# Kernel tuning notes

Measured on AMD Instinct MI355X. Metric: run time of the kernel, lower is better.

Reference implementation:

```python
import jax, jax.numpy as jnp
import numpy as np

B, N, FIN = 64, 128, 768
NFEAT, NHID, NHEADS, NCLASS = 1024, 512, 8, 512
ALPHA = 0.2
NEG_E = -9e15
NEG_S = -9e10


def setup_inputs():
    rng = np.random.RandomState(0)
    x = rng.randn(B, N, FIN).astype(np.float32)
    offset_mapping = np.zeros((B, N, 2), dtype=np.int32)
    attention_mask = np.zeros((B, N), dtype=np.float32)
    tag = np.zeros((B, N), dtype=np.float32)
    for b in range(B):
        pos, k, groups = 1, 0, 0
        n_words = int(rng.randint(30, 60))
        for _ in range(n_words):
            wl = int(rng.randint(1, 4))
            if k + wl > 120:
                break
            for _t in range(wl):
                offset_mapping[b, k] = (pos, pos + 2)  # contiguous inside word
                pos += 2
                k += 1
            pos += 1  # 1-char gap => word boundary: end == next_start - 1
            groups += 1
        groups -= 1  # last word is never closed (matches torch loop semantics)
        attention_mask[b, :groups] = 1.0
        tag[b, :groups] = (rng.rand(groups) > 0.1).astype(np.float32)
        tag[b, 0] = 1.0
    adj = (rng.rand(B, N, N) < 0.3).astype(np.float32)
    adj = np.clip(adj + np.eye(N, dtype=np.float32)[None], 0.0, 1.0)
    s = 0.02
    p = {
        'Wg_w': s * rng.randn(FIN, NFEAT), 'Wg_b': np.zeros(NFEAT),
        'hW_w': s * rng.randn(NHEADS, NFEAT, NHID), 'hW_b': np.zeros((NHEADS, NHID)),
        'ha_w': s * rng.randn(NHEADS, 2 * NHID), 'ha_b': np.zeros(NHEADS),
        'oW_w': s * rng.randn(NHID * NHEADS, NCLASS), 'oW_b': np.zeros(NCLASS),
        'oa_w': s * rng.randn(2 * NCLASS), 'oa_b': np.zeros(()),
        'fin_w': s * rng.randn(NCLASS, 1), 'fin_b': np.zeros(1),
    }
    inp = {
        'x': jnp.asarray(x), 'tag': jnp.asarray(tag),
        'offset_mapping': jnp.asarray(offset_mapping),
        'attention_mask': jnp.asarray(attention_mask), 'adj': jnp.asarray(adj),
    }
    for kk, vv in p.items():
        inp[kk] = jnp.asarray(np.asarray(vv, dtype=np.float32))
    return inp


def _group_pool(x, offs):
    # Vectorized form of the offset-grouped mean pooling loop.
    zero = (offs[:, :, 0] == 0) & (offs[:, :, 1] == 0)  # padding rows
    fz = jnp.argmax(zero, axis=1)                       # first padding row (break)
    pos = jnp.arange(N)
    valid = pos[None, :] < fz[:, None]
    nxt_start = jnp.concatenate([offs[:, 1:, 0], jnp.zeros((offs.shape[0], 1), offs.dtype)], axis=1)
    boundary = valid & (offs[:, :, 1] == nxt_start - 1)
    bi = boundary.astype(jnp.int32)
    cs = jnp.cumsum(bi, axis=1)
    seg = cs - bi                 # exclusive cumsum: group id per token
    G = cs[:, -1]                 # number of closed groups per row

    def per(xb, segb, bb):
        sums = jax.ops.segment_sum(xb, segb, num_segments=N + 1)[:N]
        cnts = jax.ops.segment_sum(jnp.ones((N,), xb.dtype), segb, num_segments=N + 1)[:N]
        ends = jax.ops.segment_sum((jnp.arange(N) + 1) * bb, segb, num_segments=N + 1)[:N]
        return sums, cnts, ends

    sums, cnts, ends = jax.vmap(per)(x, seg, bi)
    g = jnp.arange(N)[None, :]
    gv = g < G[:, None]
    x_off = jnp.where(gv[..., None], sums / jnp.maximum(cnts, 1.0)[..., None], 0.0)
    starts = jnp.concatenate([jnp.zeros((offs.shape[0], 1), jnp.int32), ends[:, :-1]], axis=1)
    starts = jnp.where(gv, starts, 0)
    ends = jnp.where(gv, ends, 0)
    return x_off, jnp.stack([starts, ends], axis=-1)  # [B,N,F_in], [B,N,2]


def _expand_row(fix):
    # Flatten [start,end) ranges in order until the first [0,0] row; rest = arange.
    zr = (fix[:, 0] == 0) & (fix[:, 1] == 0)
    fz = jnp.argmax(zr)
    valid = jnp.arange(N) < fz
    lens = jnp.where(valid, fix[:, 1] - fix[:, 0], 0)
    csum = jnp.cumsum(lens)
    excl = csum - lens
    total = csum[-1]
    l = jnp.arange(N)
    k = jnp.clip(jnp.searchsorted(csum, l, side='right'), 0, N - 1)
    val = fix[k, 0] + (l - excl[k])
    return jnp.where(l < total, val, l)


def _scores(x_off, tag, attention_mask, adj, Wg_w, Wg_b, hW_w, hW_b, ha_w, ha_b, oW_w, oW_b, oa_w, oa_b, fin_w, fin_b):
    xw = x_off @ Wg_w + Wg_b                                    # [B,N,NFEAT]
    h = jnp.einsum('bnf,hfo->bhno', xw, hW_w) + hW_b[None, :, None, :]
    # e_ij = leakyrelu(a1.h_i + a2.h_j + b): decomposition of a([h_i||h_j])
    e = jax.nn.leaky_relu(
        jnp.einsum('bhno,ho->bhn', h, ha_w[:, :NHID])[:, :, :, None]
        + jnp.einsum('bhno,ho->bhn', h, ha_w[:, NHID:])[:, :, None, :]
        + ha_b[None, :, None, None], ALPHA)
    att = jax.nn.softmax(jnp.where(adj[:, None, :, :] > 0, e, NEG_E), axis=-1)
    x1 = jax.nn.elu(jnp.einsum('bhij,bhjo->bhio', att, h))
    x1 = x1.transpose(0, 2, 1, 3).reshape(x1.shape[0], N, NHEADS * NHID)
    h2 = x1 @ oW_w + oW_b
    e2 = jax.nn.leaky_relu((h2 @ oa_w[:NCLASS])[:, :, None]
                           + (h2 @ oa_w[NCLASS:])[:, None, :] + oa_b, ALPHA)
    att2 = jax.nn.softmax(jnp.where(adj > 0, e2, NEG_E), axis=-1)
    x2 = jax.nn.elu(jnp.einsum('bij,bjo->bio', att2, h2))
    logits = (x2 @ fin_w + fin_b)[..., 0]                        # [B,N]
    m = jnp.where(tag > 0, attention_mask, 0.0)
    sc = jax.nn.softmax(jnp.where(m > 0, logits * m, NEG_S), axis=1)
    summary = m.sum(axis=1)
    ii = (jnp.arange(N, 0, -1).astype(jnp.float32)[None, :] / summary[:, None]) * m
    ii = jax.nn.softmax(jnp.where(m > 0, ii, NEG_S), axis=1)
    return sc + ii


def reference(x, tag, offset_mapping, attention_mask, adj, Wg_w, Wg_b, hW_w, hW_b, ha_w, ha_b, oW_w, oW_b, oa_w, oa_b, fin_w, fin_b):
    x_off, index_group = _group_pool(x, offset_mapping)
    sc = _scores(x_off, tag, attention_mask, adj, Wg_w, Wg_b, hW_w, hW_b, ha_w, ha_b, oW_w, oW_b, oa_w, oa_b, fin_w, fin_b)
    order = jnp.argsort(-sc, axis=1)  # jax argsort is stable; matches torch stable descending
    bidx = jnp.arange(sc.shape[0])[:, None]
    fix = index_group.at[bidx, order].set(index_group)  # scatter_(dim=1) with permutation index
    return jax.vmap(_expand_row)(fix)
```

## Files before the change

### kernel.cpp

```cpp
#include <hip/hip_runtime.h>
#include <cstddef>
#include <cstdint>

#define B_ 64
#define N_ 128
#define FIN_ 768
#define NEG_E_ (-9.0e15f)
#define NEG_S_ (-9.0e10f)
#define CHUNK_ 16

typedef unsigned short u16;
typedef unsigned int u32;
typedef float f32x4 __attribute__((ext_vector_type(4)));
typedef short s16x8 __attribute__((ext_vector_type(8)));
typedef u16 u16x4 __attribute__((ext_vector_type(4)));

__device__ __forceinline__ u16 f2bf(float x) {
  u32 u = __float_as_uint(x);
  return (u16)((u + 0x7fffu + ((u >> 16) & 1u)) >> 16);
}
__device__ __forceinline__ float b2f(u16 h) {
  return __uint_as_float(((u32)h) << 16);
}

__global__ __launch_bounds__(128) void group_pool_kernel(
    const float* __restrict__ x, const int* __restrict__ offs,
    u16* __restrict__ xoh, u16* __restrict__ xol, int* __restrict__ ig)
{
  const int b = blockIdx.x;
  const int fc = blockIdx.y;
  const int tid = threadIdx.x;
  __shared__ int o0[N_], o1[N_];
  __shared__ int bnd[N_];
  __shared__ float invlen[N_];
  __shared__ int st[N_], en[N_];
  __shared__ int Gs;
  o0[tid] = offs[(b * N_ + tid) * 2 + 0];
  o1[tid] = offs[(b * N_ + tid) * 2 + 1];
  bnd[tid] = -1;
  __syncthreads();
  if (tid == 0) {
    int fz = N_;
    for (int k = 0; k < N_; ++k) { if (o0[k] == 0 && o1[k] == 0) { fz = k; break; } }
    int g = 0, prev = 0;
    for (int k = 0; k < fz; ++k) {
      int nxt = (k + 1 < N_) ? o0[k + 1] : 0;
      if (o1[k] == nxt - 1 && g < N_) {
        bnd[k] = g;
        invlen[g] = 1.0f / (float)(k + 1 - prev);
        st[g] = prev;
        en[g] = k + 1;
        prev = k + 1;
        ++g;
      }
    }
    Gs = g;
  }
  __syncthreads();
  const int G = Gs;
  const int f = fc * 128 + tid;
  const float* xb = x + (size_t)b * N_ * FIN_ + f;
  float acc = 0.0f;
  for (int k0 = 0; k0 < N_; k0 += 8) {
    float v[8];
#pragma unroll
    for (int u = 0; u < 8; ++u) v[u] = xb[(size_t)(k0 + u) * FIN_];
#pragma unroll
    for (int u = 0; u < 8; ++u) {
      acc += v[u];
      int g = bnd[k0 + u];
      if (g >= 0) {
        float mean = acc * invlen[g];
        u16 hh = f2bf(mean);
        size_t oo = ((size_t)b * N_ + g) * FIN_ + f;
        xoh[oo] = hh;
        xol[oo] = f2bf(mean - b2f(hh));
        acc = 0.0f;
      }
    }
  }
  for (int g = G; g < N_; ++g) {
    size_t oo = ((size_t)b * N_ + g) * FIN_ + f;
    xoh[oo] = 0;
    xol[oo] = 0;
  }
  if (fc == 0) {
    int g = tid;
    ig[(b * N_ + g) * 2 + 0] = (g < G) ? st[g] : 0;
    ig[(b * N_ + g) * 2 + 1] = (g < G) ? en[g] : 0;
  }
}

__global__ __launch_bounds__(256) void pack_wgT(
    const float* __restrict__ w, u16* __restrict__ th, u16* __restrict__ tl)
{
  __shared__ float t[32][33];
  const int k0 = blockIdx.x * 32, n0 = blockIdx.y * 32;
  const int r = threadIdx.x >> 3;
  const int c = (threadIdx.x & 7) * 4;
  float4 v = *(const float4*)(w + (size_t)(k0 + r) * 1024 + n0 + c);
  t[r][c] = v.x; t[r][c + 1] = v.y; t[r][c + 2] = v.z; t[r][c + 3] = v.w;
  __syncthreads();
  u16x4 hv, lv;
#pragma unroll
  for (int i = 0; i < 4; ++i) {
    float xv = t[c + i][r];
    u16 h = f2bf(xv);
    hv[i] = h; lv[i] = f2bf(xv - b2f(h));
  }
  size_t dst = (size_t)(n0 + r) * 768 + k0 + c;
  *(u16x4*)(th + dst) = hv;
  *(u16x4*)(tl + dst) = lv;
}
__global__ __launch_bounds__(256) void pack_hwT(
    const float* __restrict__ w, u16* __restrict__ th, u16* __restrict__ tl)
{
  __shared__ float t[32][33];
  const int o0 = blockIdx.x * 32, f0 = blockIdx.y * 32, hd = blockIdx.z;
  const int r = threadIdx.x >> 3;
  const int c = (threadIdx.x & 7) * 4;
  float4 v = *(const float4*)(w + ((size_t)hd * 1024 + f0 + r) * 512 + o0 + c);
  t[r][c] = v.x; t[r][c + 1] = v.y; t[r][c + 2] = v.z; t[r][c + 3] = v.w;
  __syncthreads();
  u16x4 hv, lv;
#pragma unroll
  for (int i = 0; i < 4; ++i) {
    float xv = t[c + i][r];
    u16 h = f2bf(xv);
    hv[i] = h; lv[i] = f2bf(xv - b2f(h));
  }
  size_t dst = ((size_t)hd * 512 + o0 + r) * 1024 + f0 + c;
  *(u16x4*)(th + dst) = hv;
  *(u16x4*)(tl + dst) = lv;
}
__global__ __launch_bounds__(256) void pack_owT(
    const float* __restrict__ w, u16* __restrict__ th, u16* __restrict__ tl)
{
  __shared__ float t[32][33];
  const int k0 = blockIdx.x * 32, o0 = blockIdx.y * 32;
  const int r = threadIdx.x >> 3;
  const int c = (threadIdx.x & 7) * 4;
  float4 v = *(const float4*)(w + (size_t)(k0 + r) * 512 + o0 + c);
  t[r][c] = v.x; t[r][c + 1] = v.y; t[r][c + 2] = v.z; t[r][c + 3] = v.w;
  __syncthreads();
  u16x4 hv, lv;
#pragma unroll
  for (int i = 0; i < 4; ++i) {
    float xv = t[c + i][r];
    u16 h = f2bf(xv);
    hv[i] = h; lv[i] = f2bf(xv - b2f(h));
  }
  size_t dst = (size_t)(o0 + r) * 4096 + k0 + c;
  *(u16x4*)(th + dst) = hv;
  *(u16x4*)(tl + dst) = lv;
}

__global__ __launch_bounds__(256) void mfma_split_gemm(
    const u16* __restrict__ Ah, const u16* __restrict__ Al,
    const u16* __restrict__ Bh, const u16* __restrict__ Bl,
    const float* __restrict__ bias, int bias_mode,
    u16* __restrict__ Oh, u16* __restrict__ Ol, float* __restrict__ Of,
    int out_f32, int do_elu,
    int K, int lda, int ldb,
    long long Az, long long Bz,
    int msh, long long s_mb, int nsh, long long s_nb, long long s_n,
    long long zb_s, long long zh_s, int zH)
{
  __shared__ u16 As_h[128][40];
  __shared__ u16 As_l[128][40];
  __shared__ u16 Bs_h[128][40];
  __shared__ u16 Bs_l[128][40];
  const int tid = threadIdx.x;
  const int wave = tid >> 6, lane = tid & 63;
  const int wm = (wave >> 1) * 64, wn = (wave & 1) * 64;
  const int bn = blockIdx.x * 128, bm = blockIdx.y * 128;
  const int z = blockIdx.z;
  const u16* Ahb = Ah + (long long)z * Az;
  const u16* Alb = Al + (long long)z * Az;
  const u16* Bhb = Bh + (long long)z * Bz;
  const u16* Blb = Bl + (long long)z * Bz;
  const int lm = lane & 15, lq = lane >> 4;

  const int sr = tid >> 1;
  const int sc = (tid & 1) * 16;
  const size_t ga = (size_t)(bm + sr) * lda + sc;
  const size_t gb = (size_t)(bn + sr) * ldb + sc;

  f32x4 acc[4][4];
#pragma unroll
  for (int i = 0; i < 4; ++i)
#pragma unroll
    for (int j = 0; j < 4; ++j) acc[i][j] = (f32x4){0.0f, 0.0f, 0.0f, 0.0f};

  uint4 r0, r1, r2, r3, r4, r5, r6, r7;
  r0 = *(const uint4*)(Ahb + ga);
  r1 = *(const uint4*)(Ahb + ga + 8);
  r2 = *(const uint4*)(Alb + ga);
  r3 = *(const uint4*)(Alb + ga + 8);
  r4 = *(const uint4*)(Bhb + gb);
  r5 = *(const uint4*)(Bhb + gb + 8);
  r6 = *(const uint4*)(Blb + gb);
  r7 = *(const uint4*)(Blb + gb + 8);

  for (int k0 = 0; k0 < K; k0 += 32) {
    __syncthreads();
    *(uint4*)&As_h[sr][sc] = r0;
    *(uint4*)&As_h[sr][sc + 8] = r1;
    *(uint4*)&As_l[sr][sc] = r2;
    *(uint4*)&As_l[sr][sc + 8] = r3;
    *(uint4*)&Bs_h[sr][sc] = r4;
    *(uint4*)&Bs_h[sr][sc + 8] = r5;
    *(uint4*)&Bs_l[sr][sc] = r6;
    *(uint4*)&Bs_l[sr][sc + 8] = r7;
    __syncthreads();
    int kn = k0 + 32;
    if (kn < K) {
      r0 = *(const uint4*)(Ahb + ga + kn);
      r1 = *(const uint4*)(Ahb + ga + kn + 8);
      r2 = *(const uint4*)(Alb + ga + kn);
      r3 = *(const uint4*)(Alb + ga + kn + 8);
      r4 = *(const uint4*)(Bhb + gb + kn);
      r5 = *(const uint4*)(Bhb + gb + kn + 8);
      r6 = *(const uint4*)(Blb + gb + kn);
      r7 = *(const uint4*)(Blb + gb + kn + 8);
    }
    s16x8 fa_h[4], fa_l[4], fb_h[4], fb_l[4];
#pragma unroll
    for (int t = 0; t < 4; ++t) {
      fa_h[t] = *(const s16x8*)&As_h[wm + t * 16 + lm][lq * 8];
      fa_l[t] = *(const s16x8*)&As_l[wm + t * 16 + lm][lq * 8];
      fb_h[t] = *(const s16x8*)&Bs_h[wn + t * 16 + lm][lq * 8];
      fb_l[t] = *(const s16x8*)&Bs_l[wn + t * 16 + lm][lq * 8];
    }
#pragma unroll
    for (int i = 0; i < 4; ++i)
#pragma unroll
      for (int j = 0; j < 4; ++j) {
        acc[i][j] = __builtin_amdgcn_mfma_f32_16x16x32_bf16(fa_h[i], fb_h[j], acc[i][j], 0, 0, 0);
        acc[i][j] = __builtin_amdgcn_mfma_f32_16x16x32_bf16(fa_h[i], fb_l[j], acc[i][j], 0, 0, 0);
        acc[i][j] = __builtin_amdgcn_mfma_f32_16x16x32_bf16(fa_l[i], fb_h[j], acc[i][j], 0, 0, 0);
      }
  }

  __syncthreads();
  const long long zoff = (long long)(z / zH) * zb_s + (long long)(z % zH) * zh_s;
  const int mmask = (1 << msh) - 1;
  const int nmask = (1 << nsh) - 1;
  char* lds_raw = (char*)&As_h[0][0] + wave * 4608;
  const int rn = lane >> 2;
  const int rm = (lane & 3) * 16;

  if (out_f32) {
    float* slab = (float*)lds_raw;
#pragma unroll
    for (int j = 0; j < 4; ++j) {
#pragma unroll
      for (int i = 0; i < 4; ++i) {
        int mb = bm + wm + i * 16 + lq * 4;
        int n = bn + wn + j * 16 + lm;
        f32x4 v = acc[i][j];
        if (bias_mode == 1) v += bias[n];
        else if (bias_mode == 2) { f32x4 b4 = *(const f32x4*)&bias[mb]; v += b4; }
        if (do_elu) {
          v.x = v.x > 0.0f ? v.x : expm1f(v.x);
          v.y = v.y > 0.0f ? v.y : expm1f(v.y);
          v.z = v.z > 0.0f ? v.z : expm1f(v.z);
          v.w = v.w > 0.0f ? v.w : expm1f(v.w);
        }
        *(f32x4*)&slab[lm * 68 + i * 16 + lq * 4] = v;
      }
      __syncthreads();
      int n = bn + wn + j * 16 + rn;
      int mbase = bm + wm + rm;
      long long off = (long long)(mbase >> msh) * s_mb + (mbase & mmask)
                    + (long long)(n >> nsh) * s_nb + (long long)(n & nmask) * s_n + zoff;
      const float* src = &slab[rn * 68 + rm];
      f32x4 v0 = *(const f32x4*)(src + 0);
      f32x4 v1 = *(const f32x4*)(src + 4);
      f32x4 v2 = *(const f32x4*)(src + 8);
      f32x4 v3 = *(const f32x4*)(src + 12);
      *(f32x4*)(Of + off + 0)  = v0;
      *(f32x4*)(Of + off + 4)  = v1;
      *(f32x4*)(Of + off + 8)  = v2;
      *(f32x4*)(Of + off + 12) = v3;
      __syncthreads();
    }
  } else {
    u16* slab_h = (u16*)lds_raw;
    u16* slab_l = slab_h + 16 * 72;
#pragma unroll
    for (int j = 0; j < 4; ++j) {
#pragma unroll
      for (int i = 0; i < 4; ++i) {
        int mb = bm + wm + i * 16 + lq * 4;
        int n = bn + wn + j * 16 + lm;
        f32x4 v = acc[i][j];
        if (bias_mode == 1) v += bias[n];
        else if (bias_mode == 2) { f32x4 b4 = *(const f32x4*)&bias[mb]; v += b4; }
        if (do_elu) {
          v.x = v.x > 0.0f ? v.x : expm1f(v.x);
          v.y = v.y > 0.0f ? v.y : expm1f(v.y);
          v.z = v.z > 0.0f ? v.z : expm1f(v.z);
          v.w = v.w > 0.0f ? v.w : expm1f(v.w);
        }
        u16 h0 = f2bf(v.x), h1 = f2bf(v.y), h2 = f2bf(v.z), h3 = f2bf(v.w);
        u16x4 hv = {h0, h1, h2, h3};
        u16x4 lv = {f2bf(v.x - b2f(h0)), f2bf(v.y - b2f(h1)),
                    f2bf(v.z - b2f(h2)), f2bf(v.w - b2f(h3))};
        *(u16x4*)&slab_h[lm * 72 + i * 16 + lq * 4] = hv;
        *(u16x4*)&slab_l[lm * 72 + i * 16 + lq * 4] = lv;
      }
      __syncthreads();
      int n = bn + wn + j * 16 + rn;
      int mbase = bm + wm + rm;
      long long off = (long long)(mbase >> msh) * s_mb + (mbase & mmask)
                    + (long long)(n >> nsh) * s_nb + (long long)(n & nmask) * s_n + zoff;
      const u16* sh = &slab_h[rn * 72 + rm];
      const u16* sl = &slab_l[rn * 72 + rm];
      uint4 h0 = *(const uint4*)(sh + 0);
      uint4 h1 = *(const uint4*)(sh + 8);
      uint4 l0 = *(const uint4*)(sl + 0);
      uint4 l1 = *(const uint4*)(sl + 8);
      *(uint4*)(Oh + off + 0) = h0;
      *(uint4*)(Oh + off + 8) = h1;
      *(uint4*)(Ol + off + 0) = l0;
      *(uint4*)(Ol + off + 8) = l1;
      __syncthreads();
    }
  }
}

#define G8_BUF 49152

#define STAGE_A8(T) do { const int _t = (T); if (_t < nt) {                    \
    const int _q = _t % 3;                                                     \
    _Pragma("unroll")                                                          \
    for (int rg_ = 0; rg_ < 2; ++rg_) {                                        \
      const int r_ = wave * 16 + rg_ * 8 + srow;                               \
      const u16* s_ = Asel + (size_t)(bm + r_) * lda + _t * 32 + scol;         \
      __builtin_amdgcn_global_load_lds(                                        \
          (const __attribute__((address_space(1))) void*)s_,                   \
          (__attribute__((address_space(3))) void*)(ldsb + _q * G8_BUF +       \
              (wave * 16 + rg_ * 8) * 128),                                    \
          16, 0, 0);                                                           \
    } } } while (0)

#define STAGE_B8(T, RG0) do { const int _t = (T); if (_t < nt) {               \
    const int _q = _t % 3;                                                     \
    _Pragma("unroll")                                                          \
    for (int rg_ = (RG0); rg_ < (RG0) + 2; ++rg_) {                            \
      const int r_ = wave * 32 + rg_ * 8 + srow;                               \
      const u16* s_ = Bsel + (size_t)(bn + r_) * ldb + _t * 32 + scol;         \
      __builtin_amdgcn_global_load_lds(                                        \
          (const __attribute__((address_space(1))) void*)s_,                   \
          (__attribute__((address_space(3))) void*)(ldsb + _q * G8_BUF +       \
              16384 + (wave * 32 + rg_ * 8) * 128),                            \
          16, 0, 0);                                                           \
    } } } while (0)

#define GPHASE(J, STG) do {                                                    \
    s16x8 fb0 = *(const s16x8*)(Bbase + (J) * 2048 + hbyt);                    \
    s16x8 fb1 = *(const s16x8*)(Bbase + (J) * 2048 + lbyt);                    \
    STG;                                                                       \
    __builtin_amdgcn_s_barrier();                                              \
    asm volatile("s_waitcnt lgkmcnt(0)" ::: "memory");                         \
    __builtin_amdgcn_sched_barrier(0);                                         \
    __builtin_amdgcn_s_setprio(1);                                             \
    _Pragma("unroll")                                                          \
    for (int i_ = 0; i_ < 4; ++i_) {                                           \
      acc[i_][J] = __builtin_amdgcn_mfma_f32_16x16x32_bf16(fa[i_][0], fb0, acc[i_][J], 0, 0, 0); \
      acc[i_][J] = __builtin_amdgcn_mfma_f32_16x16x32_bf16(fa[i_][0], fb1, acc[i_][J], 0, 0, 0); \
      acc[i_][J] = __builtin_amdgcn_mfma_f32_16x16x32_bf16(fa[i_][1], fb0, acc[i_][J], 0, 0, 0); \
    }                                                                          \
    __builtin_amdgcn_s_setprio(0);                                             \
  } while (0)

__global__ __launch_bounds__(512) void mfma_split_gemm8(
    const u16* __restrict__ Ah, const u16* __restrict__ Al,
    const u16* __restrict__ Bh, const u16* __restrict__ Bl,
    const float* __restrict__ bias, int bias_mode,
    u16* __restrict__ Oh, u16* __restrict__ Ol,
    int K, int lda, int ldb,
    int msh, long long s_mb, int nsh, long long s_nb, long long s_n)
{
  __shared__ __align__(128) char ldsb[3 * G8_BUF];
  const int tid = threadIdx.x;
  const int wave = tid >> 6, lane = tid & 63;
  const int wm = (wave >> 2) * 64, wn = (wave & 3) * 64;
  const int bn = blockIdx.x * 256, bm = blockIdx.y * 128;
  const int lm = lane & 15, lq = lane >> 4;
  const int nt = K >> 5;

  const int srow = lane >> 3;
  const int sl = (lane & 7) ^ srow;
  const int scol = (sl & 3) * 8;
  const u16* Asel = (sl < 4) ? Ah : Al;
  const u16* Bsel = (sl < 4) ? Bh : Bl;

  const int hbyt = (lq ^ (lm & 7)) * 16;
  const int lbyt = hbyt ^ 64;

  f32x4 acc[4][4];
#pragma unroll
  for (int i = 0; i < 4; ++i)
#pragma unroll
    for (int j = 0; j < 4; ++j) acc[i][j] = (f32x4){0.0f, 0.0f, 0.0f, 0.0f};

  STAGE_A8(0); STAGE_B8(0, 0); STAGE_B8(0, 2);
  STAGE_A8(1); STAGE_B8(1, 0); STAGE_B8(1, 2);
  if (nt > 1) asm volatile("s_waitcnt vmcnt(6)" ::: "memory");
  else        asm volatile("s_waitcnt vmcnt(0)" ::: "memory");
  __builtin_amdgcn_s_barrier();

  for (int t = 0; t < nt; ++t) {
    const int q = t % 3;
    const char* Abase = ldsb + q * G8_BUF + (wm + lm) * 128;
    const char* Bbase = ldsb + q * G8_BUF + 16384 + (wn + lm) * 128;
    s16x8 fa[4][2];
#pragma unroll
    for (int i = 0; i < 4; ++i) {
      fa[i][0] = *(const s16x8*)(Abase + i * 2048 + hbyt);
      fa[i][1] = *(const s16x8*)(Abase + i * 2048 + lbyt);
    }
    GPHASE(0, (void)0);
    __builtin_amdgcn_s_barrier();
    GPHASE(1, STAGE_A8(t + 2));
    __builtin_amdgcn_s_barrier();
    GPHASE(2, STAGE_B8(t + 2, 0));
    __builtin_amdgcn_s_barrier();
    GPHASE(3, STAGE_B8(t + 2, 2));
    if (t + 1 < nt) {
      if (t + 2 < nt) asm volatile("s_waitcnt vmcnt(6)" ::: "memory");
      else            asm volatile("s_waitcnt vmcnt(0)" ::: "memory");
      __builtin_amdgcn_s_barrier();
    }
  }

  __syncthreads();
  const int mmask = (1 << msh) - 1;
  const int nmask = (1 << nsh) - 1;
  char* lds_raw = ldsb + wave * 4608;
  const int rn = lane >> 2;
  const int rm = (lane & 3) * 16;
  u16* slab_h = (u16*)lds_raw;
  u16* slab_l = slab_h + 16 * 72;
#pragma unroll
  for (int j = 0; j < 4; ++j) {
#pragma unroll
    for (int i = 0; i < 4; ++i) {
      int mb = bm + wm + i * 16 + lq * 4;
      int n = bn + wn + j * 16 + lm;
      f32x4 v = acc[i][j];
      if (bias_mode == 1) v += bias[n];
      else if (bias_mode == 2) { f32x4 b4 = *(const f32x4*)&bias[mb]; v += b4; }
      u16 h0 = f2bf(v.x), h1 = f2bf(v.y), h2 = f2bf(v.z), h3 = f2bf(v.w);
      u16x4 hv = {h0, h1, h2, h3};
      u16x4 lv = {f2bf(v.x - b2f(h0)), f2bf(v.y - b2f(h1)),
                  f2bf(v.z - b2f(h2)), f2bf(v.w - b2f(h3))};
      *(u16x4*)&slab_h[lm * 72 + i * 16 + lq * 4] = hv;
      *(u16x4*)&slab_l[lm * 72 + i * 16 + lq * 4] = lv;
    }
    __syncthreads();
    int n = bn + wn + j * 16 + rn;
    int mbase = bm + wm + rm;
    long long off = (long long)(mbase >> msh) * s_mb + (mbase & mmask)
                  + (long long)(n >> nsh) * s_nb + (long long)(n & nmask) * s_n;
    const u16* sh = &slab_h[rn * 72 + rm];
    const u16* slp = &slab_l[rn * 72 + rm];
    uint4 h0 = *(const uint4*)(sh + 0);
    uint4 h1 = *(const uint4*)(sh + 8);
    uint4 l0 = *(const uint4*)(slp + 0);
    uint4 l1 = *(const uint4*)(slp + 8);
    *(uint4*)(Oh + off + 0) = h0;
    *(uint4*)(Oh + off + 8) = h1;
    *(uint4*)(Ol + off + 0) = l0;
    *(uint4*)(Ol + off + 8) = l1;
    __syncthreads();
  }
}

__global__ __launch_bounds__(256) void reduce4_bias(
    const float* __restrict__ ps, const float* __restrict__ bias,
    float* __restrict__ h2T, int col0)
{
  int base = (blockIdx.x * 256 + threadIdx.x) * 4;
  int o = base >> 11, m = base & 2047;
  f32x4 v = *(const f32x4*)(ps + base);
  v += *(const f32x4*)(ps + base + 1048576);
  v += *(const f32x4*)(ps + base + 2097152);
  v += *(const f32x4*)(ps + base + 3145728);
  v += bias[o];
  *(f32x4*)(h2T + (size_t)o * 8192 + col0 + m) = v;
}

__global__ __launch_bounds__(512) void dot_pairs_hT(
    const u16* __restrict__ hTh, const u16* __restrict__ hTl,
    const float* __restrict__ W,
    float* __restrict__ esrc, float* __restrict__ edst)
{
  int bh = blockIdx.x;
  int head = bh & 7;
  int tid = threadIdx.x;
  int os = tid >> 7, i = tid & 127;
  const u16* ph = hTh + (size_t)bh * 65536 + (size_t)os * 16384 + i;
  const u16* pl = hTl + (size_t)bh * 65536 + (size_t)os * 16384 + i;
  const float* w1 = W + head * 1024 + os * 128;
  float s1 = 0.0f, s2 = 0.0f;
#pragma unroll 8
  for (int o = 0; o < 128; ++o) {
    float hv = b2f(ph[o * 128]) + b2f(pl[o * 128]);
    s1 = fmaf(hv, w1[o], s1);
    s2 = fmaf(hv, w1[512 + o], s2);
  }
  __shared__ float sh1[4][128], sh2[4][128];
  sh1[os][i] = s1;
  sh2[os][i] = s2;
  __syncthreads();
  if (os == 0) {
    esrc[bh * 128 + i] = sh1[0][i] + sh1[1][i] + sh1[2][i] + sh1[3][i];
    edst[bh * 128 + i] = sh2[0][i] + sh2[1][i] + sh2[2][i] + sh2[3][i];
  }
}

__global__ __launch_bounds__(512) void dot_pairs_h2T(
    const float* __restrict__ h2T, const float* __restrict__ oa,
    float* __restrict__ e2s, float* __restrict__ e2d)
{
  int b = blockIdx.x;
  int tid = threadIdx.x;
  int os = tid >> 7, i = tid & 127;
  const float* hb = h2T + (size_t)os * 128 * 8192 + b * 128 + i;
  const float* oa1 = oa + os * 128;
  float s1 = 0.0f, s2 = 0.0f;
#pragma unroll 8
  for (int o = 0; o < 128; ++o) {
    float hv = hb[(size_t)o * 8192];
    s1 = fmaf(hv, oa1[o], s1);
    s2 = fmaf(hv, oa1[512 + o], s2);
  }
  __shared__ float sh1[4][128], sh2[4][128];
  sh1[os][i] = s1;
  sh2[os][i] = s2;
  __syncthreads();
  if (os == 0) {
    e2s[b * 128 + i] = sh1[0][i] + sh1[1][i] + sh1[2][i] + sh1[3][i];
    e2d[b * 128 + i] = sh2[0][i] + sh2[1][i] + sh2[2][i] + sh2[3][i];
  }
}

__global__ __launch_bounds__(64) void edge_softmax_kernel(
    const float* __restrict__ esrc, const float* __restrict__ edst,
    const float* __restrict__ bias, const float* __restrict__ adj,
    float* __restrict__ attf, u16* __restrict__ atth, u16* __restrict__ attl,
    int H, int split)
{
  int row = blockIdx.x;
  int lane = threadIdx.x;
  int i = row & 127;
  int bh = row >> 7;
  int hd = bh % H;
  int b = bh / H;
  float es = esrc[row] + bias[hd];
  const float* adjr = adj + ((size_t)b * N_ + i) * N_;
  const float* edr = edst + (size_t)bh * N_;
  float v[2];
#pragma unroll
  for (int t = 0; t < 2; ++t) {
    int j = lane + t * 64;
    float e = es + edr[j];
    e = (e >= 0.0f) ? e : 0.2f * e;
    v[t] = (adjr[j] > 0.0f) ? e : NEG_E_;
  }
  float mx = fmaxf(v[0], v[1]);
  for (int off = 32; off; off >>= 1) mx = fmaxf(mx, __shfl_xor(mx, off));
  float e0 = expf(v[0] - mx), e1 = expf(v[1] - mx);
  float sm = e0 + e1;
  for (int off = 32; off; off >>= 1) sm += __shfl_xor(sm, off);
  float inv = 1.0f / sm;
  float p0 = e0 * inv, p1 = e1 * inv;
  size_t base = (size_t)row * N_;
  if (split) {
    u16 h0 = f2bf(p0), h1 = f2bf(p1);
    atth[base + lane] = h0;
    attl[base + lane] = f2bf(p0 - b2f(h0));
    atth[base + lane + 64] = h1;
    attl[base + lane + 64] = f2bf(p1 - b2f(h1));
  } else {
    attf[base + lane] = p0;
    attf[base + lane + 64] = p1;
  }
}

__global__ __launch_bounds__(256) void bgemm_elu_bt_f32(
    const float* __restrict__ A, const float* __restrict__ BT,
    float* __restrict__ C)
{
  __shared__ float As[16][64];
  __shared__ float Bs[16][68];
  const int tid = threadIdx.x;
  const int tm = blockIdx.x >> 3, tn = blockIdx.x & 7;
  const int bm = tm * 64, bn = tn * 64;
  const int b = blockIdx.y;
  const float* Ab = A + (size_t)b * 16384;
  const float* BTb = BT + (size_t)b * 128;
  const int ty = tid >> 4, tx = tid & 15;
  const int ar = tid >> 2, ac = (tid & 3) * 4;
  float acc[4][4];
#pragma unroll
  for (int i = 0; i < 4; ++i)
#pragma unroll
    for (int j = 0; j < 4; ++j) acc[i][j] = 0.0f;

  for (int k0 = 0; k0 < 128; k0 += 16) {
    float4 av = *(const float4*)(Ab + (size_t)(bm + ar) * 128 + k0 + ac);
    float4 bv = *(const float4*)(BTb + (size_t)(bn + ar) * 8192 + k0 + ac);
    __syncthreads();
    As[ac + 0][ar] = av.x; As[ac + 1][ar] = av.y; As[ac + 2][ar] = av.z; As[ac + 3][ar] = av.w;
    Bs[ac + 0][ar] = bv.x; Bs[ac + 1][ar] = bv.y; Bs[ac + 2][ar] = bv.z; Bs[ac + 3][ar] = bv.w;
    __syncthreads();
#pragma unroll
    for (int kk = 0; kk < 16; ++kk) {
      float a[4], bb[4];
      *(float4*)a  = *(const float4*)&As[kk][ty * 4];
      *(float4*)bb = *(const float4*)&Bs[kk][tx * 4];
#pragma unroll
      for (int i = 0; i < 4; ++i)
#pragma unroll
        for (int j = 0; j < 4; ++j)
          acc[i][j] = fmaf(a[i], bb[j], acc[i][j]);
    }
  }
#pragma unroll
  for (int i = 0; i < 4; ++i) {
    int row = b * 128 + bm + ty * 4 + i;
    float4 v;
    v.x = acc[i][0] > 0.0f ? acc[i][0] : expm1f(acc[i][0]);
    v.y = acc[i][1] > 0.0f ? acc[i][1] : expm1f(acc[i][1]);
    v.z = acc[i][2] > 0.0f ? acc[i][2] : expm1f(acc[i][2]);
    v.w = acc[i][3] > 0.0f ? acc[i][3] : expm1f(acc[i][3]);
    *(float4*)(C + (size_t)row * 512 + bn + tx * 4) = v;
  }
}

__global__ __launch_bounds__(256) void logits_kernel(
    const float* __restrict__ X, const float* __restrict__ w,
    const float* __restrict__ bptr, float* __restrict__ out, int R)
{
  int wv = (blockIdx.x * 256 + threadIdx.x) >> 6;
  int lane = threadIdx.x & 63;
  if (wv >= R) return;
  const float* xr = X + (size_t)wv * 512;
  float s = 0.0f;
#pragma unroll
  for (int i = 0; i < 8; ++i) {
    int c = lane + i * 64;
    s = fmaf(xr[c], w[c], s);
  }
  for (int off = 32; off; off >>= 1) s += __shfl_down(s, off);
  if (lane == 0) out[wv] = s + bptr[0];
}

__global__ __launch_bounds__(128) void finalize_kernel(
    const float* __restrict__ logits, const float* __restrict__ tag,
    const float* __restrict__ amask, const int* __restrict__ ig,
    int* __restrict__ out)
{
  const int b = blockIdx.x, tid = threadIdx.x;
  __shared__ float red[N_];
  __shared__ float scs[N_];
  __shared__ int fs[N_], fe[N_], lens[N_], csum[N_];
  __shared__ int redi[N_];

  float lg = logits[b * N_ + tid];
  float tg = tag[b * N_ + tid];
  float am = amask[b * N_ + tid];
  float m = (tg > 0.0f) ? am : 0.0f;

  float in1 = (m > 0.0f) ? lg * m : NEG_S_;
  red[tid] = in1; __syncthreads();
  for (int s = 64; s > 0; s >>= 1) { if (tid < s) red[tid] = fmaxf(red[tid], red[tid + s]); __syncthreads(); }
  float M1 = red[0]; __syncthreads();
  float e1 = expf(in1 - M1);
  red[tid] = e1; __syncthreads();
  for (int s = 64; s > 0; s >>= 1) { if (tid < s) red[tid] += red[tid + s]; __syncthreads(); }
  float S1 = red[0]; __syncthreads();
  float sc = e1 / S1;

  red[tid] = m; __syncthreads();
  for (int s = 64; s > 0; s >>= 1) { if (tid < s) red[tid] += red[tid + s]; __syncthreads(); }
  float SM = red[0]; __syncthreads();

  float in2 = (m > 0.0f) ? ((float)(N_ - tid) / SM) * m : NEG_S_;
  red[tid] = in2; __syncthreads();
  for (int s = 64; s > 0; s >>= 1) { if (tid < s) red[tid] = fmaxf(red[tid], red[tid + s]); __syncthreads(); }
  float M2 = red[0]; __syncthreads();
  float e2 = expf(in2 - M2);
  red[tid] = e2; __syncthreads();
  for (int s = 64; s > 0; s >>= 1) { if (tid < s) red[tid] += red[tid + s]; __syncthreads(); }
  float S2 = red[0]; __syncthreads();
  float ii = e2 / S2;

  scs[tid] = sc + ii;
  __syncthreads();

  float si = scs[tid];
  int rank = 0;
  for (int j = 0; j < N_; ++j) {
    float sj = scs[j];
    rank += (sj > si) || (sj == si && j < tid);
  }
  fs[tid] = ig[(b * N_ + rank) * 2 + 0];
  fe[tid] = ig[(b * N_ + rank) * 2 + 1];
  __syncthreads();

  redi[tid] = (fs[tid] == 0 && fe[tid] == 0) ? tid : N_;
  __syncthreads();
  for (int s = 64; s > 0; s >>= 1) { if (tid < s) redi[tid] = min(redi[tid], redi[tid + s]); __syncthreads(); }
  int fz = redi[0]; __syncthreads();
  lens[tid] = (tid < fz) ? (fe[tid] - fs[tid]) : 0;
  __syncthreads();
  if (tid == 0) {
    int r = 0;
    for (int k = 0; k < N_; ++k) { r += lens[k]; csum[k] = r; }
  }
  __syncthreads();
  int total = csum[N_ - 1];
  int l = tid;
  int k = 0;
  while (k < N_ && csum[k] <= l) ++k;
  if (k > N_ - 1) k = N_ - 1;
  int val = fs[k] + (l - (csum[k] - lens[k]));
  out[b * N_ + l] = (l < total) ? val : l;
}

extern "C" void kernel_launch(void* const* d_in, const int* in_sizes, int n_in,
                              void* d_out, int out_size, void* d_ws, size_t ws_size,
                              hipStream_t stream)
{
  const float* x     = (const float*)d_in[0];
  const float* tag   = (const float*)d_in[1];
  const int*   offs  = (const int*)  d_in[2];
  const float* amask = (const float*)d_in[3];
  const float* adj   = (const float*)d_in[4];
  const float* Wg_w  = (const float*)d_in[5];
  const float* Wg_b  = (const float*)d_in[6];
  const float* hW_w  = (const float*)d_in[7];
  const float* hW_b  = (const float*)d_in[8];
  const float* ha_w  = (const float*)d_in[9];
  const float* ha_b  = (const float*)d_in[10];
  const float* oW_w  = (const float*)d_in[11];
  const float* oW_b  = (const float*)d_in[12];
  const float* oa_w  = (const float*)d_in[13];
  const float* oa_b  = (const float*)d_in[14];
  const float* fin_w = (const float*)d_in[15];
  const float* fin_b = (const float*)d_in[16];
  int* out = (int*)d_out;

  char* ws = (char*)d_ws;
  size_t o = 0;
  int* ig     = (int*)(ws + o);  o += 131072;
  u16* WgT_h  = (u16*)(ws + o);  o += 1572864;
  u16* WgT_l  = (u16*)(ws + o);  o += 1572864;
  u16* hWT_h  = (u16*)(ws + o);  o += 8388608;
  u16* hWT_l  = (u16*)(ws + o);  o += 8388608;
  u16* oWT_h  = (u16*)(ws + o);  o += 4194304;
  u16* oWT_l  = (u16*)(ws + o);  o += 4194304;
  float* h2T  = (float*)(ws + o); o += 16777216;
  float* esrc = (float*)(ws + o); o += 65536;
  float* edst = (float*)(ws + o); o += 65536;
  float* e2s  = (float*)(ws + o); o += 32768;
  float* e2d  = (float*)(ws + o); o += 32768;
  float* lgts = (float*)(ws + o); o += 32768;
  u16* xw_h   = (u16*)(ws + o);  o += 16777216;
  u16* xw_l   = (u16*)(ws + o);  o += 16777216;
  char* pool  = ws + o;          o += 75497472;

  u16* xoff_h = (u16*)(pool + 0);
  u16* xoff_l = (u16*)(pool + 12582912);
  u16* hT_h   = (u16*)(pool + 0);
  u16* hT_l   = (u16*)(pool + 16777216);
  u16* x1_h   = (u16*)(pool + 33554432);
  u16* x1_l   = (u16*)(pool + 50331648);
  u16* att_h  = (u16*)(pool + 67108864);
  u16* att_l  = (u16*)(pool + 71303168);
  float* ps   = (float*)(pool + 0);
  float* att2 = (float*)(pool + 0);
  float* x2   = (float*)(pool + 4194304);

  pack_wgT<<<dim3(24, 32), 256, 0, stream>>>(Wg_w, WgT_h, WgT_l);
  pack_hwT<<<dim3(16, 32, 8), 256, 0, stream>>>(hW_w, hWT_h, hWT_l);
  pack_owT<<<dim3(128, 16), 256, 0, stream>>>(oW_w, oWT_h, oWT_l);

  group_pool_kernel<<<dim3(B_, 6), 128, 0, stream>>>(x, offs, xoff_h, xoff_l, ig);

  mfma_split_gemm8<<<dim3(32, 8), 512, 0, stream>>>(
      WgT_h, WgT_l, xoff_h, xoff_l, Wg_b, 2,
      xw_h, xw_l,
      768, 768, 768,
      10, 0, 13, 0, 1024);

  for (int b0 = 0; b0 < B_; b0 += CHUNK_) {
    mfma_split_gemm8<<<dim3(16, 16), 512, 0, stream>>>(
        xw_h + (size_t)b0 * 131072, xw_l + (size_t)b0 * 131072,
        hWT_h, hWT_l, hW_b, 1,
        hT_h, hT_l,
        1024, 1024, 1024,
        7, 524288, 9, 65536, 128);

    dot_pairs_hT<<<CHUNK_ * 8, 512, 0, stream>>>(hT_h, hT_l, ha_w, esrc, edst);
    edge_softmax_kernel<<<CHUNK_ * 8 * 128, 64, 0, stream>>>(
        esrc, edst, ha_b, adj + (size_t)b0 * 16384, nullptr, att_h, att_l, 8, 1);

    mfma_split_gemm<<<dim3(1, 4, CHUNK_ * 8), 256, 0, stream>>>(
        hT_h, hT_l, att_h, att_l, nullptr, 0,
        x1_h, x1_l, nullptr, 0, 1,
        128, 128, 128, 65536, 16384,
        9, 0, 7, 0, 4096, 524288, 512, 8);

    mfma_split_gemm<<<dim3(4, 16, 4), 256, 0, stream>>>(
        x1_h, x1_l, oWT_h, oWT_l, nullptr, 0,
        nullptr, nullptr, ps, 1, 0,
        1024, 4096, 4096, 1024, 1024,
        13, 0, 9, 0, 2048, 0, 1048576, 4);
    reduce4_bias<<<1024, 256, 0, stream>>>(ps, oW_b, h2T, b0 * 128);
  }

  dot_pairs_h2T<<<64, 512, 0, stream>>>(h2T, oa_w, e2s, e2d);
  edge_softmax_kernel<<<8192, 64, 0, stream>>>(e2s, e2d, oa_b, adj,
      att2, nullptr, nullptr, 1, 0);
  bgemm_elu_bt_f32<<<dim3(16, 64), 256, 0, stream>>>(att2, h2T, x2);

  logits_kernel<<<2048, 256, 0, stream>>>(x2, fin_w, fin_b, lgts, 8192);
  finalize_kernel<<<B_, 128, 0, stream>>>(lgts, tag, amask, ig, out);
}
```

Baseline: 855.9 us.

## Flatten GEMM main loop into one prefetch-then-compute phase per K tile

Result: faster. 831.1 us (-2.9%).

```diff
diff --git a/kernel.cpp b/kernel.cpp
--- a/kernel.cpp
+++ b/kernel.cpp
@@ -335,47 +335,28 @@
 #define STAGE_A8(T) do { const int _t = (T); if (_t < nt) {                    \
     const int _q = _t % 3;                                                     \
     _Pragma("unroll")                                                          \
-    for (int rg_ = 0; rg_ < 2; ++rg_) {                                        \
-      const int r_ = wave * 16 + rg_ * 8 + srow;                               \
-      const u16* s_ = Asel + (size_t)(bm + r_) * lda + _t * 32 + scol;         \
+    for (int rg_ = 0; rg_ < 2; ++rg_)                                          \
       __builtin_amdgcn_global_load_lds(                                        \
-          (const __attribute__((address_space(1))) void*)s_,                   \
-          (__attribute__((address_space(3))) void*)(ldsb + _q * G8_BUF +       \
-              (wave * 16 + rg_ * 8) * 128),                                    \
+          (const __attribute__((address_space(1))) void*)(gA +                 \
+              (size_t)_t * 32 + (size_t)rg_ * 8 * lda),                        \
+          (__attribute__((address_space(3))) void*)(ldsAd + _q * G8_BUF +      \
+              rg_ * 1024),                                                     \
           16, 0, 0);                                                           \
-    } } } while (0)
-
-#define STAGE_B8(T, RG0) do { const int _t = (T); if (_t < nt) {               \
+  } } while (0)
+
+#define STAGE_B8(T) do { const int _t = (T); if (_t < nt) {                    \
     const int _q = _t % 3;                                                     \
     _Pragma("unroll")                                                          \
-    for (int rg_ = (RG0); rg_ < (RG0) + 2; ++rg_) {                            \
-      const int r_ = wave * 32 + rg_ * 8 + srow;                               \
-      const u16* s_ = Bsel + (size_t)(bn + r_) * ldb + _t * 32 + scol;         \
+    for (int rg_ = 0; rg_ < 4; ++rg_)                                          \
       __builtin_amdgcn_global_load_lds(                                        \
-          (const __attribute__((address_space(1))) void*)s_,                   \
-          (__attribute__((address_space(3))) void*)(ldsb + _q * G8_BUF +       \
-              16384 + (wave * 32 + rg_ * 8) * 128),                            \
+          (const __attribute__((address_space(1))) void*)(gB +                 \
+              (size_t)_t * 32 + (size_t)rg_ * 8 * ldb),                        \
+          (__attribute__((address_space(3))) void*)(ldsBd + _q * G8_BUF +      \
+              rg_ * 1024),                                                     \
           16, 0, 0);                                                           \
-    } } } while (0)
-
-#define GPHASE(J, STG) do {                                                    \
-    s16x8 fb0 = *(const s16x8*)(Bbase + (J) * 2048 + hbyt);                    \
-    s16x8 fb1 = *(const s16x8*)(Bbase + (J) * 2048 + lbyt);                    \
-    STG;                                                                       \
-    __builtin_amdgcn_s_barrier();                                              \
-    asm volatile("s_waitcnt lgkmcnt(0)" ::: "memory");                         \
-    __builtin_amdgcn_sched_barrier(0);                                         \
-    __builtin_amdgcn_s_setprio(1);                                             \
-    _Pragma("unroll")                                                          \
-    for (int i_ = 0; i_ < 4; ++i_) {                                           \
-      acc[i_][J] = __builtin_amdgcn_mfma_f32_16x16x32_bf16(fa[i_][0], fb0, acc[i_][J], 0, 0, 0); \
-      acc[i_][J] = __builtin_amdgcn_mfma_f32_16x16x32_bf16(fa[i_][0], fb1, acc[i_][J], 0, 0, 0); \
-      acc[i_][J] = __builtin_amdgcn_mfma_f32_16x16x32_bf16(fa[i_][1], fb0, acc[i_][J], 0, 0, 0); \
-    }                                                                          \
-    __builtin_amdgcn_s_setprio(0);                                             \
-  } while (0)
-
-__global__ __launch_bounds__(512) void mfma_split_gemm8(
+  } } while (0)
+
+__global__ __launch_bounds__(512, 2) void mfma_split_gemm8(
     const u16* __restrict__ Ah, const u16* __restrict__ Al,
     const u16* __restrict__ Bh, const u16* __restrict__ Bl,
     const float* __restrict__ bias, int bias_mode,
@@ -397,6 +378,11 @@
   const u16* Asel = (sl < 4) ? Ah : Al;
   const u16* Bsel = (sl < 4) ? Bh : Bl;
 
+  const u16* gA = Asel + (size_t)(bm + wave * 16 + srow) * lda + scol;
+  const u16* gB = Bsel + (size_t)(bn + wave * 32 + srow) * ldb + scol;
+  char* ldsAd = ldsb + wave * 2048;
+  char* ldsBd = ldsb + 16384 + wave * 4096;
+
   const int hbyt = (lq ^ (lm & 7)) * 16;
   const int lbyt = hbyt ^ 64;
 
@@ -406,33 +392,43 @@
 #pragma unroll
     for (int j = 0; j < 4; ++j) acc[i][j] = (f32x4){0.0f, 0.0f, 0.0f, 0.0f};
 
-  STAGE_A8(0); STAGE_B8(0, 0); STAGE_B8(0, 2);
-  STAGE_A8(1); STAGE_B8(1, 0); STAGE_B8(1, 2);
+  STAGE_A8(0); STAGE_B8(0);
+  STAGE_A8(1); STAGE_B8(1);
   if (nt > 1) asm volatile("s_waitcnt vmcnt(6)" ::: "memory");
   else        asm volatile("s_waitcnt vmcnt(0)" ::: "memory");
   __builtin_amdgcn_s_barrier();
-
+  __builtin_amdgcn_sched_barrier(0);
+
+#pragma unroll 3
   for (int t = 0; t < nt; ++t) {
     const int q = t % 3;
+    STAGE_A8(t + 2);
+    STAGE_B8(t + 2);
     const char* Abase = ldsb + q * G8_BUF + (wm + lm) * 128;
     const char* Bbase = ldsb + q * G8_BUF + 16384 + (wn + lm) * 128;
-    s16x8 fa[4][2];
+    s16x8 fa[4][2], fb[4][2];
 #pragma unroll
     for (int i = 0; i < 4; ++i) {
+      fb[i][0] = *(const s16x8*)(Bbase + i * 2048 + hbyt);
+      fb[i][1] = *(const s16x8*)(Bbase + i * 2048 + lbyt);
       fa[i][0] = *(const s16x8*)(Abase + i * 2048 + hbyt);
       fa[i][1] = *(const s16x8*)(Abase + i * 2048 + lbyt);
     }
-    GPHASE(0, (void)0);
-    __builtin_amdgcn_s_barrier();
-    GPHASE(1, STAGE_A8(t + 2));
-    __builtin_amdgcn_s_barrier();
-    GPHASE(2, STAGE_B8(t + 2, 0));
-    __builtin_amdgcn_s_barrier();
-    GPHASE(3, STAGE_B8(t + 2, 2));
+    __builtin_amdgcn_s_setprio(1);
+#pragma unroll
+    for (int i = 0; i < 4; ++i)
+#pragma unroll
+      for (int j = 0; j < 4; ++j) {
+        acc[i][j] = __builtin_amdgcn_mfma_f32_16x16x32_bf16(fa[i][0], fb[j][0], acc[i][j], 0, 0, 0);
+        acc[i][j] = __builtin_amdgcn_mfma_f32_16x16x32_bf16(fa[i][0], fb[j][1], acc[i][j], 0, 0, 0);
+        acc[i][j] = __builtin_amdgcn_mfma_f32_16x16x32_bf16(fa[i][1], fb[j][0], acc[i][j], 0, 0, 0);
+      }
+    __builtin_amdgcn_s_setprio(0);
     if (t + 1 < nt) {
       if (t + 2 < nt) asm volatile("s_waitcnt vmcnt(6)" ::: "memory");
       else            asm volatile("s_waitcnt vmcnt(0)" ::: "memory");
       __builtin_amdgcn_s_barrier();
+      __builtin_amdgcn_sched_barrier(0);
     }
   }
 
```
